# Kernel optimization log

Measured on AMD Instinct MI355X. Metric: run time of the kernel, lower is better.

Reference implementation:

```python
import jax, jax.numpy as jnp
import numpy as np

IN_FEATURES = 768
OUT_FEATURES = 768
D_ATTN = 64


def setup_inputs() -> dict:
    key = jax.random.key(0)
    k_x, k_w1, k_b1, k_w2, k_b2 = jax.random.split(key, 5)
    x = jax.random.normal(k_x, (32, 64, 64, IN_FEATURES), dtype=jnp.float32)
    # nn.Linear(in, out): weight [out, in], bias [out]
    s1 = 1.0 / np.sqrt(IN_FEATURES)
    W1 = jax.random.uniform(k_w1, (3 * D_ATTN, IN_FEATURES), jnp.float32, -s1, s1)
    b1 = jax.random.uniform(k_b1, (3 * D_ATTN,), jnp.float32, -s1, s1)
    s2 = 1.0 / np.sqrt(D_ATTN)
    W2 = jax.random.uniform(k_w2, (OUT_FEATURES, D_ATTN), jnp.float32, -s2, s2)
    b2 = jax.random.uniform(k_b2, (OUT_FEATURES,), jnp.float32, -s2, s2)
    return {"x": x, "W1": W1, "b1": b1, "W2": W2, "b2": b2}


def reference(x, W1, b1, W2, b2) -> jnp.ndarray:
    # proj1: [b,s,n,in] -> [b,s,n,3*d_attn], then chunk into q,k,v
    qkv = jnp.einsum('bsni,oi->bsno', x, W1) + b1
    q, k, v = jnp.split(qkv, 3, axis=-1)
    # scaled dot-product attention over the n axis within each (b,s) window
    w = jnp.einsum('bsnd,bsmd->bsnm', q, k)
    a = jax.nn.softmax(w / jnp.sqrt(jnp.float32(D_ATTN)), axis=-1)
    y = jnp.einsum('bsnm,bsmd->bsnd', a, v)
    # proj2: [b,s,n,d_attn] -> [b,s,n,out]
    return jnp.einsum('bsnd,od->bsno', y, W2) + b2
```

## Files before the change

kernel.cpp:

```cpp
#include <hip/hip_runtime.h>
#include <hip/hip_bf16.h>

typedef __attribute__((ext_vector_type(8))) short bf16x8;
typedef __attribute__((ext_vector_type(4))) short s16x4;
typedef __attribute__((ext_vector_type(4))) float f32x4;

#define XBUF(b)   ((b) * 16384)
#define QK_SH     16384
#define QKS       136
#define LDS_BYTES 50176

__device__ __forceinline__ short f2b(float f) {
    __hip_bfloat16 h = __float2bfloat16(f);
    return __builtin_bit_cast(short, h);
}

__global__ void cvt_weights(const float* __restrict__ W1, const float* __restrict__ W2,
                            short* __restrict__ w1b, short* __restrict__ w2b) {
    int i = blockIdx.x * 256 + threadIdx.x;
    if (i < 192 * 768) {
        int B = i >> 9, r = i & 511;
        int lane = r >> 3, j = r & 7;
        int g = lane >> 4, c = lane & 15;
        int ot = B / 24, k32 = B - ot * 24;
        w1b[i] = f2b(W1[(16 * ot + c) * 768 + k32 * 32 + 8 * g + j]);
    }
    if (i < 768 * 64) {
        int B = i >> 9, r = i & 511;
        int lane = r >> 3, j = r & 7;
        int g = lane >> 4, c = lane & 15;
        int u = B >> 1, half = B & 1;
        w2b[i] = f2b(W2[(16 * u + c) * 64 + half * 32 + 8 * g + j]);
    }
}

__device__ __forceinline__ void gload_lds16(const float* g, unsigned char* l) {
    __builtin_amdgcn_global_load_lds(
        (const __attribute__((address_space(1))) void*)g,
        (__attribute__((address_space(3))) void*)l, 16, 0, 0);
}

#define VMWAIT(n) asm volatile("s_waitcnt vmcnt(" #n ")" ::: "memory")

#define STAGE_CHUNK(kc, b) do {                                                     \
    _Pragma("unroll")                                                               \
    for (int j = 0; j < 4; ++j) {                                                   \
        int rr = (wid * 4 + j) * 4 + (lane >> 4);                                   \
        int ss = lane & 15;                                                         \
        const float* gsrc = xg + rr * 768 + (kc) * 64 + ((ss ^ (rr & 15)) << 2);    \
        gload_lds16(gsrc, &L[XBUF(b) + (wid * 4 + j) * 1024]);                      \
    }                                                                               \
} while (0)

#define WPREF(kc, W) do {                                                           \
    _Pragma("unroll")                                                               \
    for (int ks = 0; ks < 2; ++ks)                                                  \
        _Pragma("unroll")                                                           \
        for (int oi = 0; oi < 3; ++oi)                                              \
            W[ks*3+oi] = *(const bf16x8*)(W1b +                                     \
                ((wid + 4*oi) * 24 + (kc)*2 + ks) * 512 + lane * 8);                \
} while (0)

#define COMPUTE(kc, b, W) do {                                                      \
    const unsigned char* Lb = &L[XBUF(b)];                                          \
    _Pragma("unroll")                                                               \
    for (int ks = 0; ks < 2; ++ks) {                                                \
        bf16x8 a[4];                                                                \
        _Pragma("unroll")                                                           \
        for (int rt = 0; rt < 4; ++rt) {                                            \
            int r = 16*rt + c;                                                      \
            int s0 = (8*ks + 2*g) ^ (r & 15);                                       \
            int s1 = (8*ks + 2*g + 1) ^ (r & 15);                                   \
            f32x4 lo = *(const f32x4*)(Lb + r*256 + s0*16);                         \
            f32x4 hi = *(const f32x4*)(Lb + r*256 + s1*16);                         \
            a[rt][0]=f2b(lo[0]); a[rt][1]=f2b(lo[1]);                               \
            a[rt][2]=f2b(lo[2]); a[rt][3]=f2b(lo[3]);                               \
            a[rt][4]=f2b(hi[0]); a[rt][5]=f2b(hi[1]);                               \
            a[rt][6]=f2b(hi[2]); a[rt][7]=f2b(hi[3]);                               \
        }                                                                           \
        _Pragma("unroll")                                                           \
        for (int oi = 0; oi < 3; ++oi)                                              \
            _Pragma("unroll")                                                       \
            for (int rt = 0; rt < 4; ++rt)                                          \
                acc1[rt*3+oi] = __builtin_amdgcn_mfma_f32_16x16x32_bf16(            \
                    a[rt], W[ks*3+oi], acc1[rt*3+oi], 0, 0, 0);                     \
    }                                                                               \
} while (0)

#define PIPE_ITER(kc, b, Wc, Wn) do {                                               \
    if ((kc) != 11) { VMWAIT(10); } else { VMWAIT(6); }                             \
    __builtin_amdgcn_sched_barrier(0);                                              \
    __builtin_amdgcn_s_barrier();                                                   \
    __builtin_amdgcn_sched_barrier(0);                                              \
    COMPUTE(kc, b, Wc);                                                             \
    if ((kc) + 1 < 12) WPREF((kc)+1, Wn);                                           \
    asm volatile("s_waitcnt lgkmcnt(0)" ::: "memory");                              \
    __builtin_amdgcn_sched_barrier(0);                                              \
    __builtin_amdgcn_s_barrier();                                                   \
    __builtin_amdgcn_sched_barrier(0);                                              \
    if ((kc) + 2 < 12) STAGE_CHUNK((kc)+2, b);                                      \
} while (0)

__global__ __launch_bounds__(256, 3)
void tiny_att(const float* __restrict__ x, const float* __restrict__ b1v,
              const float* __restrict__ b2v, const short* __restrict__ W1b,
              const short* __restrict__ W2b, float* __restrict__ out) {
    __shared__ __align__(16) unsigned char L[LDS_BYTES];
    short* S = (short*)L;
    const int tid  = threadIdx.x;
    const int wid  = tid >> 6;
    const int lane = tid & 63;
    const int g    = lane >> 4;
    const int c    = lane & 15;
    const int win  = blockIdx.x;
    const float* xg = x + (size_t)win * (64 * 768);
    const f32x4 zero4 = {0.f, 0.f, 0.f, 0.f};

    f32x4 acc1[12];
    #pragma unroll
    for (int i = 0; i < 12; ++i) acc1[i] = zero4;

    bf16x8 Wa[6], Wb[6];
    STAGE_CHUNK(0, 0);
    STAGE_CHUNK(1, 1);
    WPREF(0, Wa);

    #pragma unroll 1
    for (int kc = 0; kc < 12; kc += 2) {
        PIPE_ITER(kc,     0, Wa, Wb);
        PIPE_ITER(kc + 1, 1, Wb, Wa);
    }
    __syncthreads();

    #pragma unroll
    for (int oi = 0; oi < 3; ++oi) {
        int ot = wid + 4 * oi;
        int o  = 16 * ot + c;
        float bias = b1v[o];
        #pragma unroll
        for (int rt = 0; rt < 4; ++rt) {
            f32x4 v = acc1[rt * 3 + oi];
            if (oi < 2) {
                #pragma unroll
                for (int r = 0; r < 4; ++r)
                    S[QK_SH + (16 * rt + 4 * g + r) * QKS + o] = f2b(v[r] + bias);
            } else {
                int d = o - 128;
                s16x4 sv;
                sv[0] = f2b(v[0] + bias); sv[1] = f2b(v[1] + bias);
                sv[2] = f2b(v[2] + bias); sv[3] = f2b(v[3] + bias);
                *(s16x4*)&S[d * 72 + 16 * rt + 4 * g] = sv;
            }
        }
    }
    __syncthreads();

    f32x4 sc[4];
    #pragma unroll
    for (int mt = 0; mt < 4; ++mt) sc[mt] = zero4;
    #pragma unroll
    for (int ks = 0; ks < 2; ++ks) {
        bf16x8 aq = *(const bf16x8*)&S[QK_SH + (16 * wid + c) * QKS + 32 * ks + 8 * g];
        #pragma unroll
        for (int mt = 0; mt < 4; ++mt) {
            bf16x8 bk = *(const bf16x8*)&S[QK_SH + (16 * mt + c) * QKS + 64 + 32 * ks + 8 * g];
            sc[mt] = __builtin_amdgcn_mfma_f32_16x16x32_bf16(aq, bk, sc[mt], 0, 0, 0);
        }
    }

    float p[4][4];
    const float kS = 0.125f * 1.44269504088896f;
    #pragma unroll
    for (int r = 0; r < 4; ++r) {
        float m0 = fmaxf(fmaxf(sc[0][r], sc[1][r]), fmaxf(sc[2][r], sc[3][r]));
        m0 = fmaxf(m0, __shfl_xor(m0, 1));
        m0 = fmaxf(m0, __shfl_xor(m0, 2));
        m0 = fmaxf(m0, __shfl_xor(m0, 4));
        m0 = fmaxf(m0, __shfl_xor(m0, 8));
        float s0 = 0.f;
        float pr[4];
        #pragma unroll
        for (int mt = 0; mt < 4; ++mt) { pr[mt] = exp2f((sc[mt][r] - m0) * kS); s0 += pr[mt]; }
        s0 += __shfl_xor(s0, 1);
        s0 += __shfl_xor(s0, 2);
        s0 += __shfl_xor(s0, 4);
        s0 += __shfl_xor(s0, 8);
        float inv = __builtin_amdgcn_rcpf(s0);
        #pragma unroll
        for (int mt = 0; mt < 4; ++mt) p[mt][r] = pr[mt] * inv;
    }

    const int ptb = 4608 + wid * 1280;
    #pragma unroll
    for (int mt = 0; mt < 4; ++mt) {
        s16x4 sv;
        sv[0] = f2b(p[mt][0]); sv[1] = f2b(p[mt][1]);
        sv[2] = f2b(p[mt][2]); sv[3] = f2b(p[mt][3]);
        *(s16x4*)&S[ptb + (16 * mt + c) * 20 + 4 * g] = sv;
    }

    f32x4 y4[4];
    #pragma unroll
    for (int it = 0; it < 4; ++it) y4[it] = zero4;
    #pragma unroll
    for (int ks = 0; ks < 2; ++ks) {
        bf16x8 pb;
        #pragma unroll
        for (int j = 0; j < 8; ++j)
            pb[j] = S[ptb + (32 * ks + 8 * g + j) * 20 + c];
        #pragma unroll
        for (int it = 0; it < 4; ++it) {
            bf16x8 av = *(const bf16x8*)&S[(16 * it + c) * 72 + 32 * ks + 8 * g];
            y4[it] = __builtin_amdgcn_mfma_f32_16x16x32_bf16(av, pb, y4[it], 0, 0, 0);
        }
    }
    #pragma unroll
    for (int it = 0; it < 4; ++it) {
        s16x4 sv;
        sv[0] = f2b(y4[it][0]); sv[1] = f2b(y4[it][1]);
        sv[2] = f2b(y4[it][2]); sv[3] = f2b(y4[it][3]);
        *(s16x4*)&S[ptb + c * 72 + 16 * it + 4 * g] = sv;
    }
    bf16x8 ay0 = *(const bf16x8*)&S[ptb + c * 72 + 8 * g];
    bf16x8 ay1 = *(const bf16x8*)&S[ptb + c * 72 + 32 + 8 * g];

    float* orow = out + ((size_t)win * 64 + 16 * wid + c) * 768 + 4 * g;
    #pragma unroll 4
    for (int u = 0; u < 48; ++u) {
        bf16x8 bw0 = *(const bf16x8*)(W2b + (2 * u) * 512 + lane * 8);
        bf16x8 bw1 = *(const bf16x8*)(W2b + (2 * u + 1) * 512 + lane * 8);
        f32x4 t = __builtin_amdgcn_mfma_f32_16x16x32_bf16(bw0, ay0, zero4, 0, 0, 0);
        t = __builtin_amdgcn_mfma_f32_16x16x32_bf16(bw1, ay1, t, 0, 0, 0);
        f32x4 bb = *(const f32x4*)(b2v + 16 * u + 4 * g);
        t[0] += bb[0]; t[1] += bb[1]; t[2] += bb[2]; t[3] += bb[3];
        *(f32x4*)(orow + 16 * u) = t;
    }
}

__global__ __launch_bounds__(256)
void tiny_att_fb(const float* __restrict__ x, const float* __restrict__ W1,
                 const float* __restrict__ b1, const float* __restrict__ W2,
                 const float* __restrict__ b2, float* __restrict__ out) {
    __shared__ float QKV[64][200];
    __shared__ float Y[64][64];
    const int win = blockIdx.x, tid = threadIdx.x;
    const float* xw = x + (size_t)win * 49152;
    for (int t = tid; t < 64 * 192; t += 256) {
        int n = t / 192, o = t % 192;
        float s = b1[o];
        for (int k = 0; k < 768; ++k) s += xw[n * 768 + k] * W1[o * 768 + k];
        QKV[n][o] = s;
    }
    __syncthreads();
    if (tid < 64) {
        int q = tid;
        float scr[64], m = -1e30f;
        for (int k = 0; k < 64; ++k) {
            float s = 0;
            for (int d = 0; d < 64; ++d) s += QKV[q][d] * QKV[k][64 + d];
            scr[k] = s * 0.125f; m = fmaxf(m, scr[k]);
        }
        float den = 0;
        for (int k = 0; k < 64; ++k) { scr[k] = __expf(scr[k] - m); den += scr[k]; }
        float inv = 1.f / den;
        for (int d = 0; d < 64; ++d) {
            float y = 0;
            for (int k = 0; k < 64; ++k) y += scr[k] * QKV[k][128 + d];
            Y[q][d] = y * inv;
        }
    }
    __syncthreads();
    for (int t = tid; t < 64 * 768; t += 256) {
        int n = t / 768, o = t % 768;
        float s = b2[o];
        for (int d = 0; d < 64; ++d) s += Y[n][d] * W2[o * 64 + d];
        out[(size_t)win * 49152 + t] = s;
    }
}

extern "C" void kernel_launch(void* const* d_in, const int* in_sizes, int n_in,
                              void* d_out, int out_size, void* d_ws, size_t ws_size,
                              hipStream_t stream) {
    const float* x  = (const float*)d_in[0];
    const float* W1 = (const float*)d_in[1];
    const float* b1 = (const float*)d_in[2];
    const float* W2 = (const float*)d_in[3];
    const float* b2 = (const float*)d_in[4];
    float* out = (float*)d_out;
    const int nwin = in_sizes[0] / (64 * 768);
    const size_t need = (size_t)(192 * 768 + 768 * 64) * sizeof(short);
    if (ws_size >= need) {
        short* w1b = (short*)d_ws;
        short* w2b = w1b + 192 * 768;
        cvt_weights<<<576, 256, 0, stream>>>(W1, W2, w1b, w2b);
        tiny_att<<<nwin, 256, 0, stream>>>(x, b1, b2, w1b, w2b, out);
    } else {
        tiny_att_fb<<<nwin, 256, 0, stream>>>(x, W1, b1, W2, b2, out);
    }
}
```

Before: 219.6 us.

## Process window pairs per block, overlapping proj2 of first with proj1 of second

Each block now handles two attention windows. The second half of the first window's output projection is interleaved into the second window's input-projection pipeline, so its MFMA work and stores overlap with the x loads. The x staging pipeline goes from double to triple buffering with a deeper prefetch distance. LDS is reorganised into a Q/K region, a V^T region and a scratch region. Grid size is halved, and the hand-tuned vmcnt wait counts carry a correctness risk. Per-block serial work also grows, which reduces parallelism.

```diff
diff --git a/kernel.cpp b/kernel.cpp
--- a/kernel.cpp
+++ b/kernel.cpp
@@ -6,9 +6,10 @@
 typedef __attribute__((ext_vector_type(4))) float f32x4;
 
 #define XBUF(b)   ((b) * 16384)
-#define QK_SH     16384
 #define QKS       136
-#define LDS_BYTES 50176
+#define VT_SH     8704
+#define SCR_SH    13312
+#define LDS_BYTES 49152
 
 __device__ __forceinline__ short f2b(float f) {
     __hip_bfloat16 h = __float2bfloat16(f);
@@ -42,12 +43,12 @@
 
 #define VMWAIT(n) asm volatile("s_waitcnt vmcnt(" #n ")" ::: "memory")
 
-#define STAGE_CHUNK(kc, b) do {                                                     \
+#define STAGE_CHUNK(XG, kc, b) do {                                                 \
     _Pragma("unroll")                                                               \
     for (int j = 0; j < 4; ++j) {                                                   \
         int rr = (wid * 4 + j) * 4 + (lane >> 4);                                   \
         int ss = lane & 15;                                                         \
-        const float* gsrc = xg + rr * 768 + (kc) * 64 + ((ss ^ (rr & 15)) << 2);    \
+        const float* gsrc = (XG) + rr * 768 + (kc) * 64 + ((ss ^ (rr & 15)) << 2);  \
         gload_lds16(gsrc, &L[XBUF(b) + (wid * 4 + j) * 1024]);                      \
     }                                                                               \
 } while (0)
@@ -87,8 +88,10 @@
     }                                                                               \
 } while (0)
 
-#define PIPE_ITER(kc, b, Wc, Wn) do {                                               \
-    if ((kc) != 11) { VMWAIT(10); } else { VMWAIT(6); }                             \
+#define PIPE_ITER0(XG, kc, b, Wc, Wn) do {                                          \
+    if ((kc) <= 9)       { VMWAIT(14); }                                            \
+    else if ((kc) == 10) { VMWAIT(10); }                                            \
+    else                 { VMWAIT(6);  }                                            \
     __builtin_amdgcn_sched_barrier(0);                                              \
     __builtin_amdgcn_s_barrier();                                                   \
     __builtin_amdgcn_sched_barrier(0);                                              \
@@ -98,13 +101,170 @@
     __builtin_amdgcn_sched_barrier(0);                                              \
     __builtin_amdgcn_s_barrier();                                                   \
     __builtin_amdgcn_sched_barrier(0);                                              \
-    if ((kc) + 2 < 12) STAGE_CHUNK((kc)+2, b);                                      \
+    if ((kc) + 3 < 12) STAGE_CHUNK(XG, (kc)+3, b);                                  \
+} while (0)
+
+#define PIECES(kc) do {                                                             \
+    _Pragma("unroll")                                                               \
+    for (int q = 0; q < 2; ++q) {                                                   \
+        int u = 24 + 2 * (kc) + q;                                                  \
+        f32x4 t = __builtin_amdgcn_mfma_f32_16x16x32_bf16(ay0w0, P2[2*q], zero4, 0, 0, 0); \
+        t = __builtin_amdgcn_mfma_f32_16x16x32_bf16(ay1w0, P2[2*q+1], t, 0, 0, 0);  \
+        _Pragma("unroll")                                                           \
+        for (int r = 0; r < 4; ++r)                                                 \
+            orow0[(size_t)(4 * g + r) * 768 + 16 * u + c] = t[r] + b2r[q];          \
+    }                                                                               \
+} while (0)
+
+#define P2LOAD(kc) do {                                                             \
+    _Pragma("unroll")                                                               \
+    for (int q = 0; q < 2; ++q) {                                                   \
+        int u = 24 + 2 * (kc) + q;                                                  \
+        P2[2*q]   = *(const bf16x8*)(W2b + (2*u) * 512 + lane * 8);                 \
+        P2[2*q+1] = *(const bf16x8*)(W2b + (2*u+1) * 512 + lane * 8);               \
+        b2r[q] = b2v[16 * u + c];                                                   \
+    }                                                                               \
+} while (0)
+
+#define PIPE_ITER1(XG, kc, b, Wc, Wn) do {                                          \
+    if ((kc) == 0)       { VMWAIT(20); }                                            \
+    else if ((kc) == 1)  { VMWAIT(40); }                                            \
+    else if ((kc) == 10) { VMWAIT(44); }                                            \
+    else if ((kc) == 11) { VMWAIT(40); }                                            \
+    else                 { VMWAIT(48); }                                            \
+    __builtin_amdgcn_sched_barrier(0);                                              \
+    __builtin_amdgcn_s_barrier();                                                   \
+    __builtin_amdgcn_sched_barrier(0);                                              \
+    COMPUTE(kc, b, Wc);                                                             \
+    PIECES(kc);                                                                     \
+    if ((kc) + 1 < 12) P2LOAD((kc)+1);                                              \
+    if ((kc) + 1 < 12) WPREF((kc)+1, Wn);                                           \
+    asm volatile("s_waitcnt lgkmcnt(0)" ::: "memory");                              \
+    __builtin_amdgcn_sched_barrier(0);                                              \
+    __builtin_amdgcn_s_barrier();                                                   \
+    __builtin_amdgcn_sched_barrier(0);                                              \
+    if ((kc) + 3 < 12) STAGE_CHUNK(XG, (kc)+3, b);                                  \
+} while (0)
+
+#define DO_ATTN(AY0, AY1) do {                                                      \
+    __syncthreads();                                                                \
+    _Pragma("unroll")                                                               \
+    for (int oi = 0; oi < 3; ++oi) {                                                \
+        int ot = wid + 4 * oi;                                                      \
+        int o  = 16 * ot + c;                                                       \
+        float bias = b1v[o];                                                        \
+        _Pragma("unroll")                                                           \
+        for (int rt = 0; rt < 4; ++rt) {                                            \
+            f32x4 v = acc1[rt * 3 + oi];                                            \
+            if (oi < 2) {                                                           \
+                _Pragma("unroll")                                                   \
+                for (int r = 0; r < 4; ++r)                                         \
+                    S[(16 * rt + 4 * g + r) * QKS + o] = f2b(v[r] + bias);          \
+            } else {                                                                \
+                int d = o - 128;                                                    \
+                s16x4 sv;                                                           \
+                sv[0] = f2b(v[0] + bias); sv[1] = f2b(v[1] + bias);                 \
+                sv[2] = f2b(v[2] + bias); sv[3] = f2b(v[3] + bias);                 \
+                *(s16x4*)&S[VT_SH + d * 72 + 16 * rt + 4 * g] = sv;                 \
+            }                                                                       \
+        }                                                                           \
+    }                                                                               \
+    __syncthreads();                                                                \
+    f32x4 sc[4];                                                                    \
+    _Pragma("unroll")                                                               \
+    for (int mt = 0; mt < 4; ++mt) sc[mt] = zero4;                                  \
+    _Pragma("unroll")                                                               \
+    for (int ks = 0; ks < 2; ++ks) {                                                \
+        bf16x8 aq = *(const bf16x8*)&S[(16 * wid + c) * QKS + 32 * ks + 8 * g];     \
+        _Pragma("unroll")                                                           \
+        for (int mt = 0; mt < 4; ++mt) {                                            \
+            bf16x8 bk = *(const bf16x8*)&S[(16 * mt + c) * QKS + 64 + 32 * ks + 8 * g]; \
+            sc[mt] = __builtin_amdgcn_mfma_f32_16x16x32_bf16(aq, bk, sc[mt], 0, 0, 0); \
+        }                                                                           \
+    }                                                                               \
+    float p[4][4];                                                                  \
+    const float kS = 0.125f * 1.44269504088896f;                                    \
+    _Pragma("unroll")                                                               \
+    for (int r = 0; r < 4; ++r) {                                                   \
+        float m0 = fmaxf(fmaxf(sc[0][r], sc[1][r]), fmaxf(sc[2][r], sc[3][r]));     \
+        m0 = fmaxf(m0, __shfl_xor(m0, 1));                                          \
+        m0 = fmaxf(m0, __shfl_xor(m0, 2));                                          \
+        m0 = fmaxf(m0, __shfl_xor(m0, 4));                                          \
+        m0 = fmaxf(m0, __shfl_xor(m0, 8));                                          \
+        float s0 = 0.f, pr[4];                                                      \
+        _Pragma("unroll")                                                           \
+        for (int mt = 0; mt < 4; ++mt) { pr[mt] = exp2f((sc[mt][r] - m0) * kS); s0 += pr[mt]; } \
+        s0 += __shfl_xor(s0, 1);                                                    \
+        s0 += __shfl_xor(s0, 2);                                                    \
+        s0 += __shfl_xor(s0, 4);                                                    \
+        s0 += __shfl_xor(s0, 8);                                                    \
+        float inv = __builtin_amdgcn_rcpf(s0);                                      \
+        _Pragma("unroll")                                                           \
+        for (int mt = 0; mt < 4; ++mt) p[mt][r] = pr[mt] * inv;                     \
+    }                                                                               \
+    const int ptb = SCR_SH + wid * 1280;                                            \
+    _Pragma("unroll")                                                               \
+    for (int mt = 0; mt < 4; ++mt) {                                                \
+        s16x4 sv;                                                                   \
+        sv[0] = f2b(p[mt][0]); sv[1] = f2b(p[mt][1]);                               \
+        sv[2] = f2b(p[mt][2]); sv[3] = f2b(p[mt][3]);                               \
+        *(s16x4*)&S[ptb + (16 * mt + c) * 20 + 4 * g] = sv;                         \
+    }                                                                               \
+    f32x4 y4[4];                                                                    \
+    _Pragma("unroll")                                                               \
+    for (int it = 0; it < 4; ++it) y4[it] = zero4;                                  \
+    _Pragma("unroll")                                                               \
+    for (int ks = 0; ks < 2; ++ks) {                                                \
+        bf16x8 pb;                                                                  \
+        _Pragma("unroll")                                                           \
+        for (int j = 0; j < 8; ++j)                                                 \
+            pb[j] = S[ptb + (32 * ks + 8 * g + j) * 20 + c];                        \
+        _Pragma("unroll")                                                           \
+        for (int it = 0; it < 4; ++it) {                                            \
+            bf16x8 av = *(const bf16x8*)&S[VT_SH + (16 * it + c) * 72 + 32 * ks + 8 * g]; \
+            y4[it] = __builtin_amdgcn_mfma_f32_16x16x32_bf16(av, pb, y4[it], 0, 0, 0); \
+        }                                                                           \
+    }                                                                               \
+    _Pragma("unroll")                                                               \
+    for (int it = 0; it < 4; ++it) {                                                \
+        s16x4 sv;                                                                   \
+        sv[0] = f2b(y4[it][0]); sv[1] = f2b(y4[it][1]);                             \
+        sv[2] = f2b(y4[it][2]); sv[3] = f2b(y4[it][3]);                             \
+        *(s16x4*)&S[ptb + c * 72 + 16 * it + 4 * g] = sv;                           \
+    }                                                                               \
+    AY0 = *(const bf16x8*)&S[ptb + c * 72 + 8 * g];                                 \
+    AY1 = *(const bf16x8*)&S[ptb + c * 72 + 32 + 8 * g];                            \
+} while (0)
+
+#define PROJ2_CHUNKS(CH0, CH1, AY0, AY1, OROW) do {                                 \
+    _Pragma("unroll 1")                                                             \
+    for (int ch = (CH0); ch < (CH1); ++ch) {                                        \
+        f32x4 a2[8];                                                                \
+        _Pragma("unroll")                                                           \
+        for (int i = 0; i < 8; ++i) a2[i] = zero4;                                  \
+        _Pragma("unroll")                                                           \
+        for (int oi = 0; oi < 8; ++oi) {                                            \
+            int u = ch * 8 + oi;                                                    \
+            bf16x8 bw0 = *(const bf16x8*)(W2b + (2 * u) * 512 + lane * 8);          \
+            a2[oi] = __builtin_amdgcn_mfma_f32_16x16x32_bf16(AY0, bw0, a2[oi], 0, 0, 0); \
+            bf16x8 bw1 = *(const bf16x8*)(W2b + (2 * u + 1) * 512 + lane * 8);      \
+            a2[oi] = __builtin_amdgcn_mfma_f32_16x16x32_bf16(AY1, bw1, a2[oi], 0, 0, 0); \
+        }                                                                           \
+        _Pragma("unroll")                                                           \
+        for (int oi = 0; oi < 8; ++oi) {                                            \
+            int o = 16 * (ch * 8 + oi) + c;                                         \
+            float bias = b2v[o];                                                    \
+            _Pragma("unroll")                                                       \
+            for (int r = 0; r < 4; ++r)                                             \
+                (OROW)[(size_t)(4 * g + r) * 768 + o] = a2[oi][r] + bias;           \
+        }                                                                           \
+    }                                                                               \
 } while (0)
 
 __global__ __launch_bounds__(256, 3)
-void tiny_att(const float* __restrict__ x, const float* __restrict__ b1v,
-              const float* __restrict__ b2v, const short* __restrict__ W1b,
-              const short* __restrict__ W2b, float* __restrict__ out) {
+void tiny_att_pair(const float* __restrict__ x, const float* __restrict__ b1v,
+                   const float* __restrict__ b2v, const short* __restrict__ W1b,
+                   const short* __restrict__ W2b, float* __restrict__ out, int nwin) {
     __shared__ __align__(16) unsigned char L[LDS_BYTES];
     short* S = (short*)L;
     const int tid  = threadIdx.x;
@@ -112,129 +272,77 @@
     const int lane = tid & 63;
     const int g    = lane >> 4;
     const int c    = lane & 15;
-    const int win  = blockIdx.x;
-    const float* xg = x + (size_t)win * (64 * 768);
+    const int w0   = blockIdx.x * 2;
+    if (w0 >= nwin) return;
+    const bool has2 = (w0 + 1) < nwin;
+    const float* xg0 = x + (size_t)w0 * 49152;
+    const float* xg1 = xg0 + 49152;
+    float* orow0 = out + ((size_t)w0 * 64 + 16 * wid) * 768;
     const f32x4 zero4 = {0.f, 0.f, 0.f, 0.f};
 
+    bf16x8 Wa[6], Wb[6];
     f32x4 acc1[12];
+    bf16x8 ay0w0, ay1w0;
+
     #pragma unroll
     for (int i = 0; i < 12; ++i) acc1[i] = zero4;
-
-    bf16x8 Wa[6], Wb[6];
-    STAGE_CHUNK(0, 0);
-    STAGE_CHUNK(1, 1);
-    WPREF(0, Wa);
-
-    #pragma unroll 1
-    for (int kc = 0; kc < 12; kc += 2) {
-        PIPE_ITER(kc,     0, Wa, Wb);
-        PIPE_ITER(kc + 1, 1, Wb, Wa);
-    }
+    {
+        const float* xg = xg0;
+        STAGE_CHUNK(xg, 0, 0);
+        STAGE_CHUNK(xg, 1, 1);
+        STAGE_CHUNK(xg, 2, 2);
+        WPREF(0, Wa);
+        PIPE_ITER0(xg, 0,  0, Wa, Wb);
+        PIPE_ITER0(xg, 1,  1, Wb, Wa);
+        PIPE_ITER0(xg, 2,  2, Wa, Wb);
+        PIPE_ITER0(xg, 3,  0, Wb, Wa);
+        PIPE_ITER0(xg, 4,  1, Wa, Wb);
+        PIPE_ITER0(xg, 5,  2, Wb, Wa);
+        PIPE_ITER0(xg, 6,  0, Wa, Wb);
+        PIPE_ITER0(xg, 7,  1, Wb, Wa);
+        PIPE_ITER0(xg, 8,  2, Wa, Wb);
+        PIPE_ITER0(xg, 9,  0, Wb, Wa);
+        PIPE_ITER0(xg, 10, 1, Wa, Wb);
+        PIPE_ITER0(xg, 11, 2, Wb, Wa);
+    }
+    DO_ATTN(ay0w0, ay1w0);
     __syncthreads();
 
+    if (!has2) {
+        PROJ2_CHUNKS(0, 6, ay0w0, ay1w0, orow0);
+        return;
+    }
+
+    PROJ2_CHUNKS(0, 3, ay0w0, ay1w0, orow0);
+
+    bf16x8 P2[4];
+    float b2r[2];
     #pragma unroll
-    for (int oi = 0; oi < 3; ++oi) {
-        int ot = wid + 4 * oi;
-        int o  = 16 * ot + c;
-        float bias = b1v[o];
-        #pragma unroll
-        for (int rt = 0; rt < 4; ++rt) {
-            f32x4 v = acc1[rt * 3 + oi];
-            if (oi < 2) {
-                #pragma unroll
-                for (int r = 0; r < 4; ++r)
-                    S[QK_SH + (16 * rt + 4 * g + r) * QKS + o] = f2b(v[r] + bias);
-            } else {
-                int d = o - 128;
-                s16x4 sv;
-                sv[0] = f2b(v[0] + bias); sv[1] = f2b(v[1] + bias);
-                sv[2] = f2b(v[2] + bias); sv[3] = f2b(v[3] + bias);
-                *(s16x4*)&S[d * 72 + 16 * rt + 4 * g] = sv;
-            }
-        }
-    }
-    __syncthreads();
-
-    f32x4 sc[4];
-    #pragma unroll
-    for (int mt = 0; mt < 4; ++mt) sc[mt] = zero4;
-    #pragma unroll
-    for (int ks = 0; ks < 2; ++ks) {
-        bf16x8 aq = *(const bf16x8*)&S[QK_SH + (16 * wid + c) * QKS + 32 * ks + 8 * g];
-        #pragma unroll
-        for (int mt = 0; mt < 4; ++mt) {
-            bf16x8 bk = *(const bf16x8*)&S[QK_SH + (16 * mt + c) * QKS + 64 + 32 * ks + 8 * g];
-            sc[mt] = __builtin_amdgcn_mfma_f32_16x16x32_bf16(aq, bk, sc[mt], 0, 0, 0);
-        }
-    }
-
-    float p[4][4];
-    const float kS = 0.125f * 1.44269504088896f;
-    #pragma unroll
-    for (int r = 0; r < 4; ++r) {
-        float m0 = fmaxf(fmaxf(sc[0][r], sc[1][r]), fmaxf(sc[2][r], sc[3][r]));
-        m0 = fmaxf(m0, __shfl_xor(m0, 1));
-        m0 = fmaxf(m0, __shfl_xor(m0, 2));
-        m0 = fmaxf(m0, __shfl_xor(m0, 4));
-        m0 = fmaxf(m0, __shfl_xor(m0, 8));
-        float s0 = 0.f;
-        float pr[4];
-        #pragma unroll
-        for (int mt = 0; mt < 4; ++mt) { pr[mt] = exp2f((sc[mt][r] - m0) * kS); s0 += pr[mt]; }
-        s0 += __shfl_xor(s0, 1);
-        s0 += __shfl_xor(s0, 2);
-        s0 += __shfl_xor(s0, 4);
-        s0 += __shfl_xor(s0, 8);
-        float inv = __builtin_amdgcn_rcpf(s0);
-        #pragma unroll
-        for (int mt = 0; mt < 4; ++mt) p[mt][r] = pr[mt] * inv;
-    }
-
-    const int ptb = 4608 + wid * 1280;
-    #pragma unroll
-    for (int mt = 0; mt < 4; ++mt) {
-        s16x4 sv;
-        sv[0] = f2b(p[mt][0]); sv[1] = f2b(p[mt][1]);
-        sv[2] = f2b(p[mt][2]); sv[3] = f2b(p[mt][3]);
-        *(s16x4*)&S[ptb + (16 * mt + c) * 20 + 4 * g] = sv;
-    }
-
-    f32x4 y4[4];
-    #pragma unroll
-    for (int it = 0; it < 4; ++it) y4[it] = zero4;
-    #pragma unroll
-    for (int ks = 0; ks < 2; ++ks) {
-        bf16x8 pb;
-        #pragma unroll
-        for (int j = 0; j < 8; ++j)
-            pb[j] = S[ptb + (32 * ks + 8 * g + j) * 20 + c];
-        #pragma unroll
-        for (int it = 0; it < 4; ++it) {
-            bf16x8 av = *(const bf16x8*)&S[(16 * it + c) * 72 + 32 * ks + 8 * g];
-            y4[it] = __builtin_amdgcn_mfma_f32_16x16x32_bf16(av, pb, y4[it], 0, 0, 0);
-        }
-    }
-    #pragma unroll
-    for (int it = 0; it < 4; ++it) {
-        s16x4 sv;
-        sv[0] = f2b(y4[it][0]); sv[1] = f2b(y4[it][1]);
-        sv[2] = f2b(y4[it][2]); sv[3] = f2b(y4[it][3]);
-        *(s16x4*)&S[ptb + c * 72 + 16 * it + 4 * g] = sv;
-    }
-    bf16x8 ay0 = *(const bf16x8*)&S[ptb + c * 72 + 8 * g];
-    bf16x8 ay1 = *(const bf16x8*)&S[ptb + c * 72 + 32 + 8 * g];
-
-    float* orow = out + ((size_t)win * 64 + 16 * wid + c) * 768 + 4 * g;
-    #pragma unroll 4
-    for (int u = 0; u < 48; ++u) {
-        bf16x8 bw0 = *(const bf16x8*)(W2b + (2 * u) * 512 + lane * 8);
-        bf16x8 bw1 = *(const bf16x8*)(W2b + (2 * u + 1) * 512 + lane * 8);
-        f32x4 t = __builtin_amdgcn_mfma_f32_16x16x32_bf16(bw0, ay0, zero4, 0, 0, 0);
-        t = __builtin_amdgcn_mfma_f32_16x16x32_bf16(bw1, ay1, t, 0, 0, 0);
-        f32x4 bb = *(const f32x4*)(b2v + 16 * u + 4 * g);
-        t[0] += bb[0]; t[1] += bb[1]; t[2] += bb[2]; t[3] += bb[3];
-        *(f32x4*)(orow + 16 * u) = t;
-    }
+    for (int i = 0; i < 12; ++i) acc1[i] = zero4;
+    {
+        const float* xg = xg1;
+        STAGE_CHUNK(xg, 0, 0);
+        STAGE_CHUNK(xg, 1, 1);
+        P2LOAD(0);
+        WPREF(0, Wa);
+        STAGE_CHUNK(xg, 2, 2);
+        PIPE_ITER1(xg, 0,  0, Wa, Wb);
+        PIPE_ITER1(xg, 1,  1, Wb, Wa);
+        PIPE_ITER1(xg, 2,  2, Wa, Wb);
+        PIPE_ITER1(xg, 3,  0, Wb, Wa);
+        PIPE_ITER1(xg, 4,  1, Wa, Wb);
+        PIPE_ITER1(xg, 5,  2, Wb, Wa);
+        PIPE_ITER1(xg, 6,  0, Wa, Wb);
+        PIPE_ITER1(xg, 7,  1, Wb, Wa);
+        PIPE_ITER1(xg, 8,  2, Wa, Wb);
+        PIPE_ITER1(xg, 9,  0, Wb, Wa);
+        PIPE_ITER1(xg, 10, 1, Wa, Wb);
+        PIPE_ITER1(xg, 11, 2, Wb, Wa);
+    }
+    bf16x8 ay0w1, ay1w1;
+    DO_ATTN(ay0w1, ay1w1);
+    float* orow1 = orow0 + (size_t)64 * 768;
+    PROJ2_CHUNKS(0, 6, ay0w1, ay1w1, orow1);
 }
 
 __global__ __launch_bounds__(256)
@@ -288,12 +396,13 @@
     const float* b2 = (const float*)d_in[4];
     float* out = (float*)d_out;
     const int nwin = in_sizes[0] / (64 * 768);
+    const int npair = (nwin + 1) / 2;
     const size_t need = (size_t)(192 * 768 + 768 * 64) * sizeof(short);
     if (ws_size >= need) {
         short* w1b = (short*)d_ws;
         short* w2b = w1b + 192 * 768;
         cvt_weights<<<576, 256, 0, stream>>>(W1, W2, w1b, w2b);
-        tiny_att<<<nwin, 256, 0, stream>>>(x, b1, b2, w1b, w2b, out);
+        tiny_att_pair<<<npair, 256, 0, stream>>>(x, b1, b2, w1b, w2b, out, nwin);
     } else {
         tiny_att_fb<<<nwin, 256, 0, stream>>>(x, W1, b1, W2, b2, out);
     }
```

New measurement: 308.6 us. 40.5% more time.
